# Kernel tuning notes

Hardware: AMD Instinct MI355X
Metric: run time of the kernel (lower is better)

The kernel has to match this reference:

```python
import jax, jax.numpy as jnp
import numpy as np

N_NODES = 40000
N_EDGES = 640000
D = 128          # node_dim == edge_dim
EMB = 2 * D      # emb_dim = node_dim + edge_dim
L = 3            # n_layers
BN_EPS = 1e-5


def setup_inputs() -> dict:
    key = jax.random.key(0)
    ks = jax.random.split(key, 8)
    h = jax.random.normal(ks[0], (N_NODES, D), jnp.float32)
    e = jax.random.normal(ks[1], (N_EDGES, D), jnp.float32)
    src = jax.random.randint(ks[2], (N_EDGES,), 0, N_NODES, dtype=jnp.int32)
    dst = jax.random.randint(ks[3], (N_EDGES,), 0, N_NODES, dtype=jnp.int32)
    s = 1.0 / np.sqrt(EMB)
    W1 = jax.random.normal(ks[4], (L, EMB, EMB), jnp.float32) * s
    b1 = jnp.zeros((L, EMB), jnp.float32)
    gamma = jnp.ones((L, EMB), jnp.float32)
    beta = jnp.zeros((L, EMB), jnp.float32)
    W2 = jax.random.normal(ks[5], (L, D, EMB), jnp.float32) * s
    b2 = jnp.zeros((L, D), jnp.float32)
    return {"h": h, "e": e, "W1": W1, "b1": b1, "gamma": gamma,
            "beta": beta, "W2": W2, "b2": b2, "src": src, "dst": dst}


def _gin_forward(h, e, W1, b1, gamma, beta, W2, b2, src, dst):
    n_layers = W1.shape[0]
    n_nodes = h.shape[0]
    for l in range(n_layers):
        # gather src node feats, concat with edge feats: [E, 2D]
        x = jnp.concatenate([h[src], e], axis=1)
        # MLP: Linear -> BatchNorm (batch stats) -> ReLU -> Linear
        x = x @ W1[l].T + b1[l]
        mu = jnp.mean(x, axis=0)
        var = jnp.var(x, axis=0)
        x = (x - mu) * jax.lax.rsqrt(var + BN_EPS) * gamma[l] + beta[l]
        x = jax.nn.relu(x)
        m = x @ W2[l].T + b2[l]  # [E, D] per-edge messages
        # scatter-sum messages to destination nodes
        h = jax.ops.segment_sum(m, dst, num_segments=n_nodes)
        if l < n_layers - 1:  # non-output layers apply ReLU to h and e
            h = jax.nn.relu(h)
            e = jax.nn.relu(e)
        # dropout is identity in eval mode
    return h


def reference(h, e, W1, b1, gamma, beta, W2, b2, src, dst):
    return _gin_forward(h, e, W1, b1, gamma, beta, W2, b2, src, dst)
```

## Files before the change

kernel.cpp:

```cpp
#include <hip/hip_runtime.h>

typedef unsigned short u16;
typedef __attribute__((ext_vector_type(8))) short short8;
typedef __attribute__((ext_vector_type(4))) float f32x4;
typedef __attribute__((ext_vector_type(4))) unsigned int u32x4;

#define N_NODES 40000
#define N_EDGES 640000

__device__ __forceinline__ u16 f2bf(float f) {
  unsigned int u = __builtin_bit_cast(unsigned int, f);
  u += 0x7FFFu + ((u >> 16) & 1u);
  return (u16)(u >> 16);
}
__device__ __forceinline__ float bf2f(u16 h) {
  unsigned int u = ((unsigned int)h) << 16;
  return __builtin_bit_cast(float, u);
}
__device__ __forceinline__ short8 relu8(short8 s) {
  u32x4 w = __builtin_bit_cast(u32x4, s);
#pragma unroll
  for (int j = 0; j < 4; ++j) {
    unsigned int t = (w[j] >> 15) & 0x10001u;
    w[j] &= ~(t * 0xFFFFu);
  }
  return __builtin_bit_cast(short8, w);
}
__device__ __forceinline__ void pk_atomic_add_bf16(u16* p, float c0, float c1) {
  unsigned int pk = (unsigned int)f2bf(c0) | ((unsigned int)f2bf(c1) << 16);
  asm volatile("global_atomic_pk_add_bf16 %0, %1, off" :: "v"(p), "v"(pk) : "memory");
}

__global__ void prep_weights(const float* __restrict__ W1,
                             const float* __restrict__ W2,
                             u16* __restrict__ w1t, u16* __restrict__ w2t) {
  int gid = blockIdx.x * 256 + threadIdx.x;
  if (gid < 3 * 16 * 8 * 64) {
    int l = gid >> 13;
    int rem = gid & 8191;
    int ntg = rem >> 9;
    int ks = (rem >> 6) & 7;
    int lane = rem & 63;
    int n = ntg * 16 + (lane & 15);
    int k0 = ks * 32 + (lane >> 4) * 8;
    const float* s = W1 + l * 65536 + n * 256 + k0;
    u16* d = w1t + (size_t)gid * 8;
#pragma unroll
    for (int j = 0; j < 8; ++j) d[j] = f2bf(s[j]);
  } else if (gid < 3 * 16 * 8 * 64 + 3 * 8 * 8 * 64) {
    int g = gid - 3 * 16 * 8 * 64;
    int l = g >> 12;
    int rem = g & 4095;
    int ntg = rem >> 9;
    int ks = (rem >> 6) & 7;
    int lane = rem & 63;
    int n = ntg * 16 + (lane & 15);
    int k0 = ks * 32 + (lane >> 4) * 8;
    const float* s = W2 + l * 32768 + n * 256 + k0;
    u16* d = w2t + (size_t)g * 8;
#pragma unroll
    for (int j = 0; j < 8; ++j) d[j] = f2bf(s[j]);
  }
}

__global__ void cvt_vec(const float* __restrict__ in, u16* __restrict__ out,
                        int n8) {
  int i = blockIdx.x * 256 + threadIdx.x;
  if (i >= n8) return;
  const float4* p = reinterpret_cast<const float4*>(in) + (size_t)i * 2;
  float4 a = p[0], b = p[1];
  short8 v;
  v[0] = (short)f2bf(a.x); v[1] = (short)f2bf(a.y);
  v[2] = (short)f2bf(a.z); v[3] = (short)f2bf(a.w);
  v[4] = (short)f2bf(b.x); v[5] = (short)f2bf(b.y);
  v[6] = (short)f2bf(b.z); v[7] = (short)f2bf(b.w);
  *reinterpret_cast<short8*>(out + (size_t)i * 8) = v;
}

__global__ void hist_dst(const int* __restrict__ dst, int* __restrict__ cnt) {
  int e = blockIdx.x * 256 + threadIdx.x;
  if (e < N_EDGES) atomicAdd(&cnt[dst[e]], 1);
}

__global__ void scan_hist(const int* __restrict__ cnt, int* __restrict__ cursor) {
  __shared__ int ls[1024];
  const int tid = threadIdx.x;
  const int b = tid * 40;
  const int lim = (b < N_NODES) ? ((N_NODES - b < 40) ? (N_NODES - b) : 40) : 0;
  int s = 0;
  for (int j = 0; j < lim; ++j) s += cnt[b + j];
  ls[tid] = s;
  __syncthreads();
  for (int off = 1; off < 1024; off <<= 1) {
    int v = (tid >= off) ? ls[tid - off] : 0;
    __syncthreads();
    ls[tid] += v;
    __syncthreads();
  }
  int run = (tid == 0) ? 0 : ls[tid - 1];
  for (int j = 0; j < lim; ++j) {
    cursor[b + j] = run;
    run += cnt[b + j];
  }
}

__global__ void rank_edges(const int* __restrict__ src, const int* __restrict__ dst,
                           int* __restrict__ cursor, int* __restrict__ srcS,
                           int* __restrict__ dstS, int* __restrict__ rank) {
  int e = blockIdx.x * 256 + threadIdx.x;
  if (e >= N_EDGES) return;
  int d = dst[e];
  int r = atomicAdd(&cursor[d], 1);
  rank[e] = r;
  srcS[r] = src[e];
  dstS[r] = d;
}

__global__ void permute_e(const float* __restrict__ e, const int* __restrict__ rank,
                          u16* __restrict__ ebfS) {
  int t = blockIdx.x * 256 + threadIdx.x;
  int row = t >> 2;
  int part = t & 3;
  if (row >= N_EDGES) return;
  const float4* p = reinterpret_cast<const float4*>(e + (size_t)row * 128 + part * 32);
  u16* dp = ebfS + (size_t)rank[row] * 128 + part * 32;
#pragma unroll
  for (int j = 0; j < 4; ++j) {
    float4 a = p[j * 2], b = p[j * 2 + 1];
    short8 v;
    v[0] = (short)f2bf(a.x); v[1] = (short)f2bf(a.y);
    v[2] = (short)f2bf(a.z); v[3] = (short)f2bf(a.w);
    v[4] = (short)f2bf(b.x); v[5] = (short)f2bf(b.y);
    v[6] = (short)f2bf(b.z); v[7] = (short)f2bf(b.w);
    *(short8*)(dp + j * 8) = v;
  }
}

#define LOAD_B4(SET, KS) { _Pragma("unroll") \
  for (int nt = 0; nt < 4; ++nt) \
    SET[nt] = *(const short8*)(wbase + ((nt * 8 + (KS)) * 64 + lane) * 8); }
#define LOAD_A_LDS(ARR, SET, KS) { _Pragma("unroll") \
  for (int mt = 0; mt < 4; ++mt) \
    SET[mt] = *(const short8*)&ARR[(KS)][mt * 16 + lrow][lk * 8]; }
#define MFMA4(ACC, A, B) { _Pragma("unroll") \
  for (int nt = 0; nt < 4; ++nt) { _Pragma("unroll") \
    for (int mt = 0; mt < 4; ++mt) \
      ACC[mt][nt] = __builtin_amdgcn_mfma_f32_16x16x32_bf16(A[mt], B[nt], ACC[mt][nt], 0, 0, 0); } }

template <int RELU_E>
__global__ __launch_bounds__(256) void gin_g1(
    const u16* __restrict__ hbf, const u16* __restrict__ ebf,
    const int* __restrict__ srcS, const u16* __restrict__ w1t,
    u16* __restrict__ xout, float* __restrict__ stats) {
  __shared__ u16 sA[8][64][36];
  const int tid = threadIdx.x;
  const long e0 = (long)blockIdx.x * 64;
  const int wid = tid >> 6, lane = tid & 63;
  const int lrow = lane & 15, lk = lane >> 4;

  {
    const int row = tid >> 2, c2 = tid & 3;
    const int sr = srcS[e0 + row];
    const u16* hrow = hbf + (size_t)sr * 128 + c2 * 8;
    const u16* erow = ebf + (size_t)(e0 + row) * 128 + c2 * 8;
    short8 t0 = *(const short8*)(hrow + 0);
    short8 t1 = *(const short8*)(hrow + 32);
    short8 t2 = *(const short8*)(hrow + 64);
    short8 t3 = *(const short8*)(hrow + 96);
    short8 t4 = *(const short8*)(erow + 0);
    short8 t5 = *(const short8*)(erow + 32);
    short8 t6 = *(const short8*)(erow + 64);
    short8 t7 = *(const short8*)(erow + 96);
    if (RELU_E) { t4 = relu8(t4); t5 = relu8(t5); t6 = relu8(t6); t7 = relu8(t7); }
    *(short8*)&sA[0][row][c2 * 8] = t0;
    *(short8*)&sA[1][row][c2 * 8] = t1;
    *(short8*)&sA[2][row][c2 * 8] = t2;
    *(short8*)&sA[3][row][c2 * 8] = t3;
    *(short8*)&sA[4][row][c2 * 8] = t4;
    *(short8*)&sA[5][row][c2 * 8] = t5;
    *(short8*)&sA[6][row][c2 * 8] = t6;
    *(short8*)&sA[7][row][c2 * 8] = t7;
  }
  __syncthreads();

  f32x4 acc[4][4] = {};
  const u16* wbase = w1t + (size_t)wid * 16384;
  {
    short8 a0[4], a1[4], b0[4], b1[4];
    LOAD_A_LDS(sA, a0, 0) LOAD_B4(b0, 0)
    LOAD_A_LDS(sA, a1, 1) LOAD_B4(b1, 1)
    MFMA4(acc, a0, b0)
    LOAD_A_LDS(sA, a0, 2) LOAD_B4(b0, 2)
    MFMA4(acc, a1, b1)
    LOAD_A_LDS(sA, a1, 3) LOAD_B4(b1, 3)
    MFMA4(acc, a0, b0)
    LOAD_A_LDS(sA, a0, 4) LOAD_B4(b0, 4)
    MFMA4(acc, a1, b1)
    LOAD_A_LDS(sA, a1, 5) LOAD_B4(b1, 5)
    MFMA4(acc, a0, b0)
    LOAD_A_LDS(sA, a0, 6) LOAD_B4(b0, 6)
    MFMA4(acc, a1, b1)
    LOAD_A_LDS(sA, a1, 7) LOAD_B4(b1, 7)
    MFMA4(acc, a0, b0)
    MFMA4(acc, a1, b1)
  }

  float* statp = stats + (blockIdx.x & 63) * 512;
#pragma unroll
  for (int nt = 0; nt < 4; ++nt) {
    const int col = wid * 64 + nt * 16 + lrow;
    float sm = 0.f, sq = 0.f;
#pragma unroll
    for (int mt = 0; mt < 4; ++mt) {
#pragma unroll
      for (int i = 0; i < 4; ++i) {
        float v = acc[mt][nt][i];
        const long row = e0 + mt * 16 + lk * 4 + i;
        xout[(size_t)row * 256 + col] = f2bf(v);
        sm += v; sq += v * v;
      }
    }
    sm += __shfl_xor(sm, 16); sq += __shfl_xor(sq, 16);
    sm += __shfl_xor(sm, 32); sq += __shfl_xor(sq, 32);
    if (lk == 0) {
      atomicAdd(statp + col, sm);
      atomicAdd(statp + 256 + col, sq);
    }
  }
}

__global__ void gin_bnstats(const float* __restrict__ stats,
                            const float* __restrict__ gamma,
                            const float* __restrict__ beta,
                            float* __restrict__ ab) {
  int c = threadIdx.x;
  float sm = 0.f, sq = 0.f;
  for (int i = 0; i < 64; ++i) {
    sm += stats[i * 512 + c];
    sq += stats[i * 512 + 256 + c];
  }
  const float inv = 1.0f / (float)N_EDGES;
  float mu = sm * inv;
  float var = fmaxf(sq * inv - mu * mu, 0.f);
  float a = gamma[c] * rsqrtf(var + 1e-5f);
  ab[c] = a;
  ab[256 + c] = beta[c] - mu * a;
}

__global__ __launch_bounds__(256) void gin_scat(
    const u16* __restrict__ xin, const float* __restrict__ ab,
    const int* __restrict__ dstS, u16* __restrict__ Y) {
  const int tid = threadIdx.x;
  const long e0 = (long)blockIdx.x * 64;
  const int cp = tid & 127;
  const int half = tid >> 7;
  const int col = cp * 2;
  const int r0 = half * 32;
  const float a0 = ab[col], a1 = ab[col + 1];
  const float b0 = ab[256 + col], b1 = ab[256 + col + 1];
  float c0 = 0.f, c1 = 0.f;
  int cur = dstS[e0 + r0];
#pragma unroll 8
  for (int r = r0; r < r0 + 32; ++r) {
    unsigned int u = *(const unsigned int*)(xin + (size_t)(e0 + r) * 256 + col);
    float y0 = fmaxf(bf2f((u16)(u & 0xFFFFu)) * a0 + b0, 0.f);
    float y1 = fmaxf(bf2f((u16)(u >> 16)) * a1 + b1, 0.f);
    int d = dstS[e0 + r];
    if (d != cur) {
      pk_atomic_add_bf16(Y + (size_t)cur * 256 + col, c0, c1);
      c0 = 0.f; c1 = 0.f; cur = d;
    }
    c0 += y0; c1 += y1;
  }
  pk_atomic_add_bf16(Y + (size_t)cur * 256 + col, c0, c1);
}

template <int LAST>
__global__ __launch_bounds__(256) void gin_nodegemm(
    const u16* __restrict__ Y, const u16* __restrict__ w2t,
    const float* __restrict__ b2, const int* __restrict__ cnt,
    float* __restrict__ outf, u16* __restrict__ hbf) {
  const int tid = threadIdx.x;
  const long n0 = (long)blockIdx.x * 64;
  const int wid = tid >> 6, lane = tid & 63;
  const int lrow = lane & 15, lk = lane >> 4;
  f32x4 acc[4][2] = {};
  const u16* wb2 = w2t + (size_t)wid * 8192;
  for (int ks = 0; ks < 8; ++ks) {
    short8 af[4];
#pragma unroll
    for (int mt = 0; mt < 4; ++mt)
      af[mt] = *(const short8*)(Y + (size_t)(n0 + mt * 16 + lrow) * 256 +
                                ks * 32 + lk * 8);
#pragma unroll
    for (int nt = 0; nt < 2; ++nt) {
      short8 bf = *(const short8*)(wb2 + ((nt * 8 + ks) * 64 + lane) * 8);
#pragma unroll
      for (int mt = 0; mt < 4; ++mt)
        acc[mt][nt] =
            __builtin_amdgcn_mfma_f32_16x16x32_bf16(af[mt], bf, acc[mt][nt], 0, 0, 0);
    }
  }
  float bb[2];
#pragma unroll
  for (int nt = 0; nt < 2; ++nt) bb[nt] = b2[wid * 32 + nt * 16 + lrow];
#pragma unroll
  for (int mt = 0; mt < 4; ++mt) {
#pragma unroll
    for (int i = 0; i < 4; ++i) {
      const long node = n0 + mt * 16 + lk * 4 + i;
      const float dg = (float)cnt[node];
#pragma unroll
      for (int nt = 0; nt < 2; ++nt) {
        const int col = wid * 32 + nt * 16 + lrow;
        float v = acc[mt][nt][i] + dg * bb[nt];
        if (LAST) outf[node * 128 + col] = v;
        else      hbf[node * 128 + col] = f2bf(fmaxf(v, 0.f));
      }
    }
  }
}

extern "C" void kernel_launch(void* const* d_in, const int* in_sizes, int n_in,
                              void* d_out, int out_size, void* d_ws, size_t ws_size,
                              hipStream_t stream) {
  const float* h     = (const float*)d_in[0];
  const float* e     = (const float*)d_in[1];
  const float* W1    = (const float*)d_in[2];
  const float* gamma = (const float*)d_in[4];
  const float* beta  = (const float*)d_in[5];
  const float* W2    = (const float*)d_in[6];
  const float* b2    = (const float*)d_in[7];
  const int* src     = (const int*)d_in[8];
  const int* dst     = (const int*)d_in[9];
  float* out = (float*)d_out;

  char* ws = (char*)d_ws;
  u16*   xbuf   = (u16*)(ws);
  u16*   ebfS   = (u16*)(ws + 327680000);
  u16*   hbf    = (u16*)(ws + 491520000);
  u16*   Y      = (u16*)(ws + 501760000);
  u16*   w1t    = (u16*)(ws + 522240000);
  u16*   w2t    = (u16*)(ws + 522633216);
  float* stats  = (float*)(ws + 522829824);
  float* ab     = (float*)(ws + 522960896);
  int*   cnt    = (int*)(ws + 522962944);
  int*   cursor = (int*)(ws + 523122944);
  int*   srcS   = (int*)(ws + 523282944);
  int*   dstS   = (int*)(ws + 525842944);
  int*   rank   = (int*)(ws + 528402944);

  prep_weights<<<144, 256, 0, stream>>>(W1, W2, w1t, w2t);
  cvt_vec<<<2500, 256, 0, stream>>>(h, hbf, 640000);

  hipMemsetAsync(cnt, 0, 160000, stream);
  hist_dst<<<2500, 256, 0, stream>>>(dst, cnt);
  scan_hist<<<1, 1024, 0, stream>>>(cnt, cursor);
  rank_edges<<<2500, 256, 0, stream>>>(src, dst, cursor, srcS, dstS, rank);
  permute_e<<<10000, 256, 0, stream>>>(e, rank, ebfS);

  const int nblk = N_EDGES / 64;
  for (int l = 0; l < 3; ++l) {
    hipMemsetAsync(stats, 0, 64 * 512 * 4, stream);
    if (l == 0)
      gin_g1<0><<<nblk, 256, 0, stream>>>(hbf, ebfS, srcS, w1t, xbuf, stats);
    else
      gin_g1<1><<<nblk, 256, 0, stream>>>(hbf, ebfS, srcS,
                                          w1t + (size_t)l * 65536, xbuf, stats);
    gin_bnstats<<<1, 256, 0, stream>>>(stats, gamma + l * 256, beta + l * 256, ab);
    hipMemsetAsync(Y, 0, 20480000, stream);
    gin_scat<<<nblk, 256, 0, stream>>>(xbuf, ab, dstS, Y);
    if (l < 2)
      gin_nodegemm<0><<<625, 256, 0, stream>>>(Y, w2t + (size_t)l * 32768,
                                               b2 + l * 128, cnt, nullptr, hbf);
    else
      gin_nodegemm<1><<<625, 256, 0, stream>>>(Y, w2t + (size_t)l * 32768,
                                               b2 + l * 128, cnt, out, nullptr);
  }
}
```

Measured before the change: 1.235 ms.

## Fuse dst-segment aggregation into node GEMM via shared-memory accumulation

Replaces the per-edge atomic scatter into a global bf16 Y buffer (plus its memset) with a node-centric kernel. Each block owns 32 destination nodes, walks their dst-sorted edge range, applies BN+ReLU, accumulates in fp32 shared memory, then runs the W2 MFMA GEMM directly from shared memory. This removes atomics, the Y round trip and two launches per layer, and keeps the sums in fp32 instead of bf16. In exchange each block reads an edge range whose length depends on node degrees, so load balance varies, and the edge loads use narrow 16-bit accesses.

```diff
diff --git a/kernel.cpp b/kernel.cpp
--- a/kernel.cpp
+++ b/kernel.cpp
@@ -25,10 +25,6 @@
     w[j] &= ~(t * 0xFFFFu);
   }
   return __builtin_bit_cast(short8, w);
-}
-__device__ __forceinline__ void pk_atomic_add_bf16(u16* p, float c0, float c1) {
-  unsigned int pk = (unsigned int)f2bf(c0) | ((unsigned int)f2bf(c1) << 16);
-  asm volatile("global_atomic_pk_add_bf16 %0, %1, off" :: "v"(p), "v"(pk) : "memory");
 }
 
 __global__ void prep_weights(const float* __restrict__ W1,
@@ -247,56 +243,67 @@
   ab[256 + c] = beta[c] - mu * a;
 }
 
-__global__ __launch_bounds__(256) void gin_scat(
+template <int LAST>
+__global__ __launch_bounds__(256) void gin_agg(
     const u16* __restrict__ xin, const float* __restrict__ ab,
-    const int* __restrict__ dstS, u16* __restrict__ Y) {
+    const int* __restrict__ dstS, const int* __restrict__ cursor,
+    const int* __restrict__ cnt, const u16* __restrict__ w2t,
+    const float* __restrict__ b2, float* __restrict__ outf,
+    u16* __restrict__ hbf) {
+  __shared__ float Ya[32][258];
   const int tid = threadIdx.x;
-  const long e0 = (long)blockIdx.x * 64;
-  const int cp = tid & 127;
-  const int half = tid >> 7;
-  const int col = cp * 2;
-  const int r0 = half * 32;
-  const float a0 = ab[col], a1 = ab[col + 1];
-  const float b0 = ab[256 + col], b1 = ab[256 + col + 1];
-  float c0 = 0.f, c1 = 0.f;
-  int cur = dstS[e0 + r0];
-#pragma unroll 8
-  for (int r = r0; r < r0 + 32; ++r) {
-    unsigned int u = *(const unsigned int*)(xin + (size_t)(e0 + r) * 256 + col);
-    float y0 = fmaxf(bf2f((u16)(u & 0xFFFFu)) * a0 + b0, 0.f);
-    float y1 = fmaxf(bf2f((u16)(u >> 16)) * a1 + b1, 0.f);
-    int d = dstS[e0 + r];
-    if (d != cur) {
-      pk_atomic_add_bf16(Y + (size_t)cur * 256 + col, c0, c1);
-      c0 = 0.f; c1 = 0.f; cur = d;
-    }
-    c0 += y0; c1 += y1;
-  }
-  pk_atomic_add_bf16(Y + (size_t)cur * 256 + col, c0, c1);
-}
-
-template <int LAST>
-__global__ __launch_bounds__(256) void gin_nodegemm(
-    const u16* __restrict__ Y, const u16* __restrict__ w2t,
-    const float* __restrict__ b2, const int* __restrict__ cnt,
-    float* __restrict__ outf, u16* __restrict__ hbf) {
-  const int tid = threadIdx.x;
-  const long n0 = (long)blockIdx.x * 64;
+  const int n0 = blockIdx.x * 32;
+
+  float* yflat = &Ya[0][0];
+  for (int i = tid; i < 32 * 258; i += 256) yflat[i] = 0.f;
+  const float a0 = ab[tid];
+  const float b0 = ab[256 + tid];
+  const int rs = cursor[n0] - cnt[n0];
+  const int re = cursor[n0 + 31];
+  __syncthreads();
+
+  if (re > rs) {
+    float accr = 0.f;
+    int cur = dstS[rs];
+#pragma unroll 4
+    for (int r = rs; r < re; ++r) {
+      u16 v = xin[(size_t)r * 256 + tid];
+      int d = dstS[r];
+      float y = fmaxf(bf2f(v) * a0 + b0, 0.f);
+      if (d != cur) {
+        Ya[cur - n0][tid] += accr;
+        accr = 0.f;
+        cur = d;
+      }
+      accr += y;
+    }
+    Ya[cur - n0][tid] += accr;
+  }
+  __syncthreads();
+
   const int wid = tid >> 6, lane = tid & 63;
   const int lrow = lane & 15, lk = lane >> 4;
-  f32x4 acc[4][2] = {};
+  f32x4 acc[2][2] = {};
   const u16* wb2 = w2t + (size_t)wid * 8192;
   for (int ks = 0; ks < 8; ++ks) {
-    short8 af[4];
-#pragma unroll
-    for (int mt = 0; mt < 4; ++mt)
-      af[mt] = *(const short8*)(Y + (size_t)(n0 + mt * 16 + lrow) * 256 +
-                                ks * 32 + lk * 8);
+    short8 af[2];
+#pragma unroll
+    for (int mt = 0; mt < 2; ++mt) {
+      const float* yp = &Ya[mt * 16 + lrow][ks * 32 + lk * 8];
+      float4 f0 = *(const float4*)(yp);
+      float4 f1 = *(const float4*)(yp + 4);
+      short8 s;
+      s[0] = (short)f2bf(f0.x); s[1] = (short)f2bf(f0.y);
+      s[2] = (short)f2bf(f0.z); s[3] = (short)f2bf(f0.w);
+      s[4] = (short)f2bf(f1.x); s[5] = (short)f2bf(f1.y);
+      s[6] = (short)f2bf(f1.z); s[7] = (short)f2bf(f1.w);
+      af[mt] = s;
+    }
 #pragma unroll
     for (int nt = 0; nt < 2; ++nt) {
       short8 bf = *(const short8*)(wb2 + ((nt * 8 + ks) * 64 + lane) * 8);
 #pragma unroll
-      for (int mt = 0; mt < 4; ++mt)
+      for (int mt = 0; mt < 2; ++mt)
         acc[mt][nt] =
             __builtin_amdgcn_mfma_f32_16x16x32_bf16(af[mt], bf, acc[mt][nt], 0, 0, 0);
     }
@@ -305,7 +312,7 @@
 #pragma unroll
   for (int nt = 0; nt < 2; ++nt) bb[nt] = b2[wid * 32 + nt * 16 + lrow];
 #pragma unroll
-  for (int mt = 0; mt < 4; ++mt) {
+  for (int mt = 0; mt < 2; ++mt) {
 #pragma unroll
     for (int i = 0; i < 4; ++i) {
       const long node = n0 + mt * 16 + lk * 4 + i;
@@ -339,7 +346,6 @@
   u16*   xbuf   = (u16*)(ws);
   u16*   ebfS   = (u16*)(ws + 327680000);
   u16*   hbf    = (u16*)(ws + 491520000);
-  u16*   Y      = (u16*)(ws + 501760000);
   u16*   w1t    = (u16*)(ws + 522240000);
   u16*   w2t    = (u16*)(ws + 522633216);
   float* stats  = (float*)(ws + 522829824);
@@ -368,13 +374,13 @@
       gin_g1<1><<<nblk, 256, 0, stream>>>(hbf, ebfS, srcS,
                                           w1t + (size_t)l * 65536, xbuf, stats);
     gin_bnstats<<<1, 256, 0, stream>>>(stats, gamma + l * 256, beta + l * 256, ab);
-    hipMemsetAsync(Y, 0, 20480000, stream);
-    gin_scat<<<nblk, 256, 0, stream>>>(xbuf, ab, dstS, Y);
     if (l < 2)
-      gin_nodegemm<0><<<625, 256, 0, stream>>>(Y, w2t + (size_t)l * 32768,
-                                               b2 + l * 128, cnt, nullptr, hbf);
+      gin_agg<0><<<1250, 256, 0, stream>>>(xbuf, ab, dstS, cursor, cnt,
+                                           w2t + (size_t)l * 32768,
+                                           b2 + l * 128, nullptr, hbf);
     else
-      gin_nodegemm<1><<<625, 256, 0, stream>>>(Y, w2t + (size_t)l * 32768,
-                                               b2 + l * 128, cnt, out, nullptr);
-  }
-}
+      gin_agg<1><<<1250, 256, 0, stream>>>(xbuf, ab, dstS, cursor, cnt,
+                                           w2t + (size_t)l * 32768,
+                                           b2 + l * 128, out, nullptr);
+  }
+}
```

Result: slower. 1.672 ms (+35.4%).
